# Kernel tuning notes

Hardware: AMD Instinct MI355X
Metric: run time of the kernel (lower is better)

Reference implementation:

```python
import jax, jax.numpy as jnp
import numpy as np

B, N, M, ZD, YD, XD = 4, 512, 512, 128, 2, 1


def setup_inputs() -> dict:
    key = jax.random.key(0)
    k_t, k_z, k_x, k_w = jax.random.split(key, 4)
    return {
        "t": jax.random.normal(k_t, (B, N, XD), dtype=jnp.float32),
        "z": jax.random.normal(k_z, (B, N, ZD), dtype=jnp.float32),
        "x": jax.random.normal(k_x, (B, M, XD), dtype=jnp.float32),
        "sigma": jnp.zeros((ZD,), dtype=jnp.float32),  # log(length_scale=1) = 0
        "W": jax.random.normal(k_w, (YD, ZD), dtype=jnp.float32) * (1.0 / np.sqrt(ZD)),
        "b": jnp.zeros((YD,), dtype=jnp.float32),
    }


def reference(t, z, x, sigma, W, b):
    # diff: (b, n, m) -- sum over x_dim as in the torch code, then channelized
    diff = (x[:, None, :, :] - t[:, :, None, :]).sum(-1)
    scale = jnp.exp(sigma)  # (c,)
    # kernel: (b, n, m, c) RBF weights per channel
    kernel = jnp.exp(-0.5 * (diff[..., None] / scale) ** 2)
    # z-weighted reduction over grid points n -> (b, m, c)
    y = jnp.einsum("bnc,bnmc->bmc", z, kernel)
    # final linear: (b, m, y_dim)
    return y @ W.T + b
```

## Files before the change

### kernel.cpp

```cpp
#include <hip/hip_runtime.h>
#include <math.h>

#define B_  4
#define N_  512
#define M_  512
#define ZD_ 128
#define YD_ 2
#define XD_ 1

#define TM      8
#define NSUB    2
#define BLOCK   (NSUB * ZD_)
#define NSPLIT  8
#define NBLOCKCHUNK (N_ / NSPLIT)
#define NCHUNK  (NBLOCKCHUNK / NSUB)

#define LOG2E_HALF 0.72134752044f

__global__ __launch_bounds__(BLOCK)
void decoder_kernel(const float* __restrict__ t,
                    const float* __restrict__ z,
                    const float* __restrict__ x,
                    const float* __restrict__ sigma,
                    const float* __restrict__ W,
                    const float* __restrict__ bias,
                    float* __restrict__ out)
{
    __shared__ float2 ts2[NBLOCKCHUNK];
    __shared__ float  accs[NSUB][TM][ZD_];

    const int b   = blockIdx.y;
    const int nz  = blockIdx.z;
    const int n0  = nz * NBLOCKCHUNK;
    const int tid = threadIdx.x;
    const int sg  = tid >> 7;
    const int c   = tid & (ZD_ - 1);
    const int m0  = blockIdx.x * TM;

    if (tid < NBLOCKCHUNK) {
        const float tv = t[(size_t)b * N_ + n0 + tid];
        ts2[tid] = make_float2(tv, tv * tv);
    }
    __syncthreads();

    const float sc = __expf(sigma[c]);
    const float a2 = -LOG2E_HALF / (sc * sc);

    float Bx[TM], E[TM];
    #pragma unroll
    for (int j = 0; j < TM; ++j) {
        const float xv = x[(size_t)b * M_ + m0 + j];
        Bx[j] = -2.0f * a2 * xv;
        E[j]  = __builtin_amdgcn_exp2f(a2 * xv * xv);
    }

    const float* zp = z + ((size_t)b * N_ + n0 + sg * NCHUNK) * ZD_ + c;

    float acc[TM];
    #pragma unroll
    for (int j = 0; j < TM; ++j) acc[j] = 0.f;

    #pragma unroll 4
    for (int n = 0; n < NCHUNK; ++n) {
        const float  zv = zp[(size_t)n * ZD_];
        const float2 tt = ts2[sg * NCHUNK + n];
        const float  w  = a2 * tt.y;
        #pragma unroll
        for (int j = 0; j < TM; ++j) {
            const float p = fmaf(Bx[j], tt.x, w);
            const float e = __builtin_amdgcn_exp2f(p);
            acc[j] = fmaf(zv, e, acc[j]);
        }
    }

    #pragma unroll
    for (int j = 0; j < TM; ++j)
        accs[sg][j][c] = E[j] * acc[j];
    __syncthreads();

    {
        const int g = tid >> 5;
        const int l = tid & 31;
        float s0 = 0.f, s1 = 0.f;
        #pragma unroll
        for (int k = 0; k < 4; ++k) {
            const int cc = l + 32 * k;
            const float av = accs[0][g][cc] + accs[1][g][cc];
            s0 = fmaf(W[cc], av, s0);
            s1 = fmaf(W[ZD_ + cc], av, s1);
        }
        #pragma unroll
        for (int d = 16; d >= 1; d >>= 1) {
            s0 += __shfl_xor(s0, d);
            s1 += __shfl_xor(s1, d);
        }
        if (l == 0) {
            const float b0 = (nz == 0) ? bias[0] : 0.f;
            const float b1 = (nz == 0) ? bias[1] : 0.f;
            atomicAdd(out + ((size_t)b * M_ + m0 + g) * YD_ + 0, s0 + b0);
            atomicAdd(out + ((size_t)b * M_ + m0 + g) * YD_ + 1, s1 + b1);
        }
    }
}

extern "C" void kernel_launch(void* const* d_in, const int* in_sizes, int n_in,
                              void* d_out, int out_size, void* d_ws, size_t ws_size,
                              hipStream_t stream) {
    const float* t     = (const float*)d_in[0];
    const float* z     = (const float*)d_in[1];
    const float* x     = (const float*)d_in[2];
    const float* sigma = (const float*)d_in[3];
    const float* W     = (const float*)d_in[4];
    const float* bias  = (const float*)d_in[5];
    float* out = (float*)d_out;

    hipMemsetAsync(out, 0, (size_t)out_size * sizeof(float), stream);

    dim3 grid(M_ / TM, B_, NSPLIT);
    dim3 block(BLOCK);
    decoder_kernel<<<grid, block, 0, stream>>>(t, z, x, sigma, W, bias, out);
}
```

Measured before the change: 80.23 us.

## Register-block four channels per thread and reduce partials in registers

Each thread now owns four adjacent channels, loaded with one float4, across eight m values, and the block splits n into eight subgroups. The N split drops from 8 to 4. The exponent argument is computed directly as a2·(x−t)², so the separate E[j] factor and the t² table go away. Channel reduction against W happens in registers via wave shuffles, and only a tiny per-subgroup partial buffer goes through LDS, which cuts shared-memory traffic and atomic count. The cost is more registers per thread and fewer, larger blocks.

```diff
diff --git a/kernel.cpp b/kernel.cpp
--- a/kernel.cpp
+++ b/kernel.cpp
@@ -8,12 +8,13 @@
 #define YD_ 2
 #define XD_ 1
 
-#define TM      8
-#define NSUB    2
-#define BLOCK   (NSUB * ZD_)
-#define NSPLIT  8
-#define NBLOCKCHUNK (N_ / NSPLIT)
-#define NCHUNK  (NBLOCKCHUNK / NSUB)
+#define TM     8
+#define CQ     4
+#define NSPLIT 4
+#define NBC    (N_ / NSPLIT)
+#define NSUB   8
+#define NPT    (NBC / NSUB)
+#define BLOCK  256
 
 #define LOG2E_HALF 0.72134752044f
 
@@ -26,80 +27,90 @@
                     const float* __restrict__ bias,
                     float* __restrict__ out)
 {
-    __shared__ float2 ts2[NBLOCKCHUNK];
-    __shared__ float  accs[NSUB][TM][ZD_];
+    __shared__ float ts[NBC];
+    __shared__ float pr[NSUB][TM][YD_];
 
     const int b   = blockIdx.y;
     const int nz  = blockIdx.z;
-    const int n0  = nz * NBLOCKCHUNK;
+    const int n0  = nz * NBC;
     const int tid = threadIdx.x;
-    const int sg  = tid >> 7;
-    const int c   = tid & (ZD_ - 1);
+    const int cq  = tid & 31;
+    const int sub = tid >> 5;
+    const int c0  = cq * CQ;
     const int m0  = blockIdx.x * TM;
 
-    if (tid < NBLOCKCHUNK) {
-        const float tv = t[(size_t)b * N_ + n0 + tid];
-        ts2[tid] = make_float2(tv, tv * tv);
-    }
+    if (tid < NBC) ts[tid] = t[(size_t)b * N_ + n0 + tid];
     __syncthreads();
 
-    const float sc = __expf(sigma[c]);
-    const float a2 = -LOG2E_HALF / (sc * sc);
-
-    float Bx[TM], E[TM];
+    float a2[CQ];
     #pragma unroll
-    for (int j = 0; j < TM; ++j) {
-        const float xv = x[(size_t)b * M_ + m0 + j];
-        Bx[j] = -2.0f * a2 * xv;
-        E[j]  = __builtin_amdgcn_exp2f(a2 * xv * xv);
+    for (int k = 0; k < CQ; ++k) {
+        const float sc = __expf(sigma[c0 + k]);
+        a2[k] = -LOG2E_HALF / (sc * sc);
     }
 
-    const float* zp = z + ((size_t)b * N_ + n0 + sg * NCHUNK) * ZD_ + c;
+    float xs[TM];
+    #pragma unroll
+    for (int j = 0; j < TM; ++j)
+        xs[j] = x[(size_t)b * M_ + m0 + j];
 
-    float acc[TM];
+    const float* zp = z + ((size_t)b * N_ + n0 + sub * NPT) * ZD_ + c0;
+
+    float acc[CQ][TM];
     #pragma unroll
-    for (int j = 0; j < TM; ++j) acc[j] = 0.f;
+    for (int k = 0; k < CQ; ++k)
+        #pragma unroll
+        for (int j = 0; j < TM; ++j) acc[k][j] = 0.f;
 
-    #pragma unroll 4
-    for (int n = 0; n < NCHUNK; ++n) {
-        const float  zv = zp[(size_t)n * ZD_];
-        const float2 tt = ts2[sg * NCHUNK + n];
-        const float  w  = a2 * tt.y;
+    #pragma unroll 2
+    for (int n = 0; n < NPT; ++n) {
+        const float4 zv = *(const float4*)(zp + (size_t)n * ZD_);
+        const float  tn = ts[sub * NPT + n];
+        float u[TM];
         #pragma unroll
         for (int j = 0; j < TM; ++j) {
-            const float p = fmaf(Bx[j], tt.x, w);
-            const float e = __builtin_amdgcn_exp2f(p);
-            acc[j] = fmaf(zv, e, acc[j]);
+            const float d = xs[j] - tn;
+            u[j] = d * d;
+        }
+        const float zk[CQ] = {zv.x, zv.y, zv.z, zv.w};
+        #pragma unroll
+        for (int k = 0; k < CQ; ++k) {
+            #pragma unroll
+            for (int j = 0; j < TM; ++j) {
+                const float e = __builtin_amdgcn_exp2f(a2[k] * u[j]);
+                acc[k][j] = fmaf(zk[k], e, acc[k][j]);
+            }
         }
     }
 
     #pragma unroll
-    for (int j = 0; j < TM; ++j)
-        accs[sg][j][c] = E[j] * acc[j];
-    __syncthreads();
-
-    {
-        const int g = tid >> 5;
-        const int l = tid & 31;
+    for (int j = 0; j < TM; ++j) {
         float s0 = 0.f, s1 = 0.f;
         #pragma unroll
-        for (int k = 0; k < 4; ++k) {
-            const int cc = l + 32 * k;
-            const float av = accs[0][g][cc] + accs[1][g][cc];
-            s0 = fmaf(W[cc], av, s0);
-            s1 = fmaf(W[ZD_ + cc], av, s1);
+        for (int k = 0; k < CQ; ++k) {
+            const float av = acc[k][j];
+            s0 = fmaf(W[c0 + k],       av, s0);
+            s1 = fmaf(W[ZD_ + c0 + k], av, s1);
         }
         #pragma unroll
         for (int d = 16; d >= 1; d >>= 1) {
             s0 += __shfl_xor(s0, d);
             s1 += __shfl_xor(s1, d);
         }
-        if (l == 0) {
-            const float b0 = (nz == 0) ? bias[0] : 0.f;
-            const float b1 = (nz == 0) ? bias[1] : 0.f;
-            atomicAdd(out + ((size_t)b * M_ + m0 + g) * YD_ + 0, s0 + b0);
-            atomicAdd(out + ((size_t)b * M_ + m0 + g) * YD_ + 1, s1 + b1);
+        if (cq == 0) {
+            pr[sub][j][0] = s0;
+            pr[sub][j][1] = s1;
         }
+    }
+    __syncthreads();
+
+    if (tid < TM * YD_) {
+        const int j = tid >> 1;
+        const int y = tid & 1;
+        float s = (nz == 0) ? bias[y] : 0.f;
+        #pragma unroll
+        for (int g = 0; g < NSUB; ++g) s += pr[g][j][y];
+        atomicAdd(out + ((size_t)b * M_ + m0 + j) * YD_ + y, s);
     }
 }
 
```

Result: slower. 83.33 us (+3.9%).
